# Optimization experiments

Measured on AMD Instinct MI355X. Metric: run time of the kernel, lower is better.

## Reference

```python
import jax, jax.numpy as jnp
import numpy as np

B, LAT, FCON, NCOND = 1024, 64, 256, 1
HID, E, GATE_H = 512, 8, 64
FREC, NFUT = 256, 2
IN_SZ = LAT + FCON * NCOND          # 320
INTER = LAT + HID                   # 576
OUT_SZ = NFUT * FREC                # 512


def setup_inputs() -> dict:
    key = jax.random.key(0)
    ks = jax.random.split(key, 16)

    def kaiming(k, shape):
        # kaiming_uniform over fan_in = shape[-2] (matches torch init on [E, in, out])
        fan_in = shape[-2]
        bound = np.sqrt(6.0 / fan_in)
        return jax.random.uniform(k, shape, jnp.float32, -bound, bound)

    def lin(kw, kb, din, dout):
        bound = 1.0 / np.sqrt(din)
        w = jax.random.uniform(kw, (din, dout), jnp.float32, -bound, bound)
        b = jax.random.uniform(kb, (dout,), jnp.float32, -bound, bound)
        return w, b

    gw1, gb1 = lin(ks[0], ks[1], IN_SZ, GATE_H)
    gw2, gb2 = lin(ks[2], ks[3], GATE_H, GATE_H)
    gw3, gb3 = lin(ks[4], ks[5], GATE_H, E)

    return {
        "z": jax.random.normal(ks[6], (B, LAT), jnp.float32),
        "c": jax.random.normal(ks[7], (B, FCON * NCOND), jnp.float32),
        "w0": kaiming(ks[8], (E, IN_SZ, HID)),
        "b0": jnp.full((E, HID), 0.01, jnp.float32),
        "w1": kaiming(ks[9], (E, INTER, HID)),
        "b1": jnp.full((E, HID), 0.01, jnp.float32),
        "w2": kaiming(ks[10], (E, INTER, OUT_SZ)),
        "b2": jnp.full((E, OUT_SZ), 0.01, jnp.float32),
        "gw1": gw1, "gb1": gb1,
        "gw2": gw2, "gb2": gb2,
        "gw3": gw3, "gb3": gb3,
    }


def _moe_layer(coeff, z, layer_out, w, b, act):
    # math identical to: mixed_w = coeff @ flat(w); baddbmm(mixed_b, inp, mixed_w)
    # expressed as a fused contraction (no [B, in, out] materialization)
    inp = jnp.concatenate((z, layer_out), axis=1)          # [B, in]
    out = jnp.einsum('bi,eio,be->bo', inp, w, coeff)       # [B, out]
    out = out + coeff @ b                                  # mixed bias
    return act(out) if act is not None else out


def reference(z, c, w0, b0, w1, b1, w2, b2, gw1, gb1, gw2, gb2, gw3, gb3):
    x = jnp.concatenate((z, c), axis=1)                    # [B, IN_SZ]
    h = jax.nn.elu(x @ gw1 + gb1)
    h = jax.nn.elu(h @ gw2 + gb2)
    coeff = jax.nn.softmax(h @ gw3 + gb3, axis=1)          # [B, E]

    out = _moe_layer(coeff, z, c, w0, b0, jax.nn.elu)      # [B, HID]
    out = _moe_layer(coeff, z, out, w1, b1, jax.nn.elu)    # [B, HID]
    out = _moe_layer(coeff, z, out, w2, b2, None)          # [B, OUT_SZ]
    return out
```

## Files before the change

### kernel.cpp

```cpp
#include <hip/hip_runtime.h>
#include <hip/hip_bf16.h>
#include <stdint.h>
#include <math.h>

#define B_    1024
#define LAT   64
#define FCON  256
#define IN_SZ 320
#define HID   512
#define E_    8
#define GH    64
#define INTER 576
#define OUT_SZ 512
#define NTOT  4096
#define KI0   10
#define KI12  18

typedef __attribute__((ext_vector_type(8))) __bf16 bf16x8;
typedef __attribute__((ext_vector_type(4))) float  f32x4;

__device__ __forceinline__ float elu_f(float x) { return x > 0.f ? x : expf(x) - 1.f; }
__device__ __forceinline__ __bf16 to_bf16(float f) {
    __hip_bfloat16 h = __float2bfloat16(f);
    return *reinterpret_cast<__bf16*>(&h);
}

__device__ __forceinline__ void async_ld16(const void* g, void* l) {
    __builtin_amdgcn_global_load_lds(
        (const __attribute__((address_space(1))) unsigned int*)g,
        (__attribute__((address_space(3))) unsigned int*)l,
        16, 0, 0);
}


#define PREP_GATE 64
#define PREP_ZC   (PREP_GATE + 160)
#define PREP_W0   (PREP_ZC + 8 * KI0 * 2)
#define PREP_W1   (PREP_W0 + 8 * KI12 * 2)
#define PREP_W2   (PREP_W1 + 8 * KI12 * 2)
#define PREP_ALL  PREP_W2

#define WPAD 261
#define SMEM_F (32 * WPAD)

__device__ __forceinline__ void do_zcpack(
    int bx, const float* __restrict__ z, const float* __restrict__ c,
    bf16x8* __restrict__ Ap0, bf16x8* __restrict__ Ap1, bf16x8* __restrict__ Ap2)
{
    const int wid  = bx * 4 + (threadIdx.x >> 6);
    const int lane = threadIdx.x & 63, q = lane >> 4, r = lane & 15;
    bf16x8 v;
    if (wid < 128) {
        const int mi = wid >> 1, ki = wid & 1;
        const float* src = z + (size_t)(mi * 16 + r) * LAT + ki * 32 + q * 8;
        const f32x4 lo = *(const f32x4*)src, hi = *(const f32x4*)(src + 4);
#pragma unroll
        for (int j = 0; j < 4; j++) { v[j] = to_bf16(lo[j]); v[j + 4] = to_bf16(hi[j]); }
        Ap0[((size_t)mi * KI0  + ki) * 64 + lane] = v;
        Ap1[((size_t)mi * KI12 + ki) * 64 + lane] = v;
        Ap2[((size_t)mi * KI12 + ki) * 64 + lane] = v;
    } else {
        const int cid = wid - 128;
        const int mi = cid >> 3, ki = 2 + (cid & 7);
        const float* src = c + (size_t)(mi * 16 + r) * FCON + (ki - 2) * 32 + q * 8;
        const f32x4 lo = *(const f32x4*)src, hi = *(const f32x4*)(src + 4);
#pragma unroll
        for (int j = 0; j < 4; j++) { v[j] = to_bf16(lo[j]); v[j + 4] = to_bf16(hi[j]); }
        Ap0[((size_t)mi * KI0 + ki) * 64 + lane] = v;
    }
}

__device__ __forceinline__ void do_wpack2(
    int f, const float* __restrict__ w, bf16x8* __restrict__ Wp, int KI,
    float* __restrict__ lds)
{
    const int e = f / (2 * KI), rem = f % (2 * KI);
    const int ki = rem >> 1, ot2 = rem & 1;
    const int K = KI * 32;
    const float* base = w + ((size_t)e * K + ki * 32) * 512 + ot2 * 256;

#pragma unroll
    for (int p = 0; p < 8; ++p) {
        const int idx = p * 256 + threadIdx.x;
        const int kl = idx >> 6, c4 = idx & 63;
        const f32x4 v = *(const f32x4*)(base + (size_t)kl * 512 + c4 * 4);
        float* d = lds + kl * WPAD + c4 * 4;
        d[0] = v[0]; d[1] = v[1]; d[2] = v[2]; d[3] = v[3];
    }
    __syncthreads();

    const int wv = threadIdx.x >> 6, lane = threadIdx.x & 63;
    const int q = lane >> 4, r = lane & 15;
#pragma unroll
    for (int ff = 0; ff < 4; ++ff) {
        const int fo = wv * 4 + ff;
        const int ol = fo * 16 + r;
        bf16x8 v;
#pragma unroll
        for (int j = 0; j < 8; ++j) v[j] = to_bf16(lds[(q * 8 + j) * WPAD + ol]);
        const int ni = e * 32 + ot2 * 16 + fo;
        Wp[((size_t)ni * KI + ki) * 64 + lane] = v;
    }
}

__device__ __forceinline__ void do_gate(
    int bx, const float* __restrict__ z, const float* __restrict__ c,
    const float* __restrict__ gw1, const float* __restrict__ gb1,
    const float* __restrict__ gw2, const float* __restrict__ gb2,
    const float* __restrict__ gw3, const float* __restrict__ gb3,
    float* __restrict__ coeff, float* __restrict__ smem)
{
    float* xs = smem;
    float* h  = smem + 16 * 320;
    const int r0 = bx * 16;
    const int wave = threadIdx.x >> 6, lane = threadIdx.x & 63;

#pragma unroll
    for (int p = 0; p < 5; ++p) {
        const int idx = p * 256 + threadIdx.x;
        const int row = idx / 80, c4 = idx % 80;
        const float* src = (c4 < 16)
            ? (z + (size_t)(r0 + row) * LAT  + c4 * 4)
            : (c + (size_t)(r0 + row) * FCON + (c4 - 16) * 4);
        *(f32x4*)(xs + row * 320 + c4 * 4) = *(const f32x4*)src;
    }
    __syncthreads();

    float a0, a1, a2, a3;
    {
        const float b = gb1[lane];
        a0 = b; a1 = b; a2 = b; a3 = b;
        const float* x0 = xs + (wave * 4 + 0) * 320;
        const float* x1 = xs + (wave * 4 + 1) * 320;
        const float* x2 = xs + (wave * 4 + 2) * 320;
        const float* x3 = xs + (wave * 4 + 3) * 320;
#pragma unroll 8
        for (int i = 0; i < IN_SZ; ++i) {
            const float wv = gw1[i * GH + lane];
            a0 = fmaf(x0[i], wv, a0);
            a1 = fmaf(x1[i], wv, a1);
            a2 = fmaf(x2[i], wv, a2);
            a3 = fmaf(x3[i], wv, a3);
        }
        h[(wave * 4 + 0) * GH + lane] = elu_f(a0);
        h[(wave * 4 + 1) * GH + lane] = elu_f(a1);
        h[(wave * 4 + 2) * GH + lane] = elu_f(a2);
        h[(wave * 4 + 3) * GH + lane] = elu_f(a3);
    }
    {
        const float b = gb2[lane];
        a0 = b; a1 = b; a2 = b; a3 = b;
        const float* h0 = h + (wave * 4 + 0) * GH;
        const float* h1 = h + (wave * 4 + 1) * GH;
        const float* h2 = h + (wave * 4 + 2) * GH;
        const float* h3 = h + (wave * 4 + 3) * GH;
#pragma unroll 8
        for (int i = 0; i < GH; ++i) {
            const float wv = gw2[i * GH + lane];
            a0 = fmaf(h0[i], wv, a0);
            a1 = fmaf(h1[i], wv, a1);
            a2 = fmaf(h2[i], wv, a2);
            a3 = fmaf(h3[i], wv, a3);
        }
        h[(wave * 4 + 0) * GH + lane] = elu_f(a0);
        h[(wave * 4 + 1) * GH + lane] = elu_f(a1);
        h[(wave * 4 + 2) * GH + lane] = elu_f(a2);
        h[(wave * 4 + 3) * GH + lane] = elu_f(a3);
    }
    if (lane < 32) {
        const int rloc = lane >> 3, e = lane & 7;
        const float* hr = h + (wave * 4 + rloc) * GH;
        float lg = gb3[e];
#pragma unroll 8
        for (int i = 0; i < GH; ++i) lg = fmaf(hr[i], gw3[i * E_ + e], lg);
        float mx = lg;
        mx = fmaxf(mx, __shfl_xor(mx, 1, 8));
        mx = fmaxf(mx, __shfl_xor(mx, 2, 8));
        mx = fmaxf(mx, __shfl_xor(mx, 4, 8));
        const float ex = expf(lg - mx);
        float sm = ex;
        sm += __shfl_xor(sm, 1, 8);
        sm += __shfl_xor(sm, 2, 8);
        sm += __shfl_xor(sm, 4, 8);
        coeff[(size_t)(r0 + wave * 4 + rloc) * E_ + e] = ex / sm;
    }
}

__global__ __launch_bounds__(256) void prep_kernel(
    const float* __restrict__ z, const float* __restrict__ c,
    const float* __restrict__ w0, const float* __restrict__ w1,
    const float* __restrict__ w2,
    const float* __restrict__ gw1, const float* __restrict__ gb1,
    const float* __restrict__ gw2, const float* __restrict__ gb2,
    const float* __restrict__ gw3, const float* __restrict__ gb3,
    bf16x8* __restrict__ Ap0, bf16x8* __restrict__ Ap1, bf16x8* __restrict__ Ap2,
    bf16x8* __restrict__ Wp0, bf16x8* __restrict__ Wp1, bf16x8* __restrict__ Wp2,
    float* __restrict__ coeff)
{
    __shared__ float smem[SMEM_F];
    const int bx = blockIdx.x;
    if (bx < PREP_GATE) {
        do_gate(bx, z, c, gw1, gb1, gw2, gb2, gw3, gb3, coeff, smem);
    } else if (bx < PREP_ZC) {
        do_zcpack(bx - PREP_GATE, z, c, Ap0, Ap1, Ap2);
    } else if (bx < PREP_W0) {
        do_wpack2(bx - PREP_ZC, w0, Wp0, KI0, smem);
    } else if (bx < PREP_W1) {
        do_wpack2(bx - PREP_W0, w1, Wp1, KI12, smem);
    } else {
        do_wpack2(bx - PREP_W1, w2, Wp2, KI12, smem);
    }
}

template<int KI, int FINAL>
__global__ __launch_bounds__(256) void layer_kernel(
    const bf16x8* __restrict__ Ap, const bf16x8* __restrict__ Wp,
    const float* __restrict__ coeff, const float* __restrict__ bias,
    __bf16* __restrict__ ApN, float* __restrict__ fout)
{
    constexpr int NS = KI / 2;
    __shared__ bf16x8 bs[2][2][E_][64];
    const int lane = threadIdx.x & 63, w = threadIdx.x >> 6;
    const int q = lane >> 4, r = lane & 15;
    const int o0 = blockIdx.x * 16;
    const int nt = blockIdx.x;
    const int mi = blockIdx.y * 4 + w;

    const bf16x8* aB = Ap + (size_t)mi * KI * 64 + lane;
    const int e0 = w * 2;

    f32x4 acc[E_];
#pragma unroll
    for (int e = 0; e < E_; e++) acc[e] = (f32x4){0.f, 0.f, 0.f, 0.f};

#define STAGE(s_, buf_)                                                        \
    {                                                                          \
        _Pragma("unroll")                                                      \
        for (int kk = 0; kk < 2; ++kk) {                                       \
            _Pragma("unroll")                                                  \
            for (int t = 0; t < 2; ++t) {                                      \
                const int e = e0 + t;                                          \
                const bf16x8* g = Wp +                                         \
                    ((size_t)e * 32 * KI + (size_t)nt * KI + ((s_) * 2 + kk)) * 64 + lane; \
                async_ld16((const void*)g, (void*)&bs[buf_][kk][e][0]);        \
            }                                                                  \
        }                                                                      \
    }

    STAGE(0, 0);
    bf16x8 af0 = aB[0], af1 = aB[64];
    __syncthreads();

    int cur = 0;
#pragma unroll
    for (int s = 0; s < NS; ++s) {
        bf16x8 afn0 = af0, afn1 = af1;
        if (s + 1 < NS) {
            STAGE(s + 1, cur ^ 1);
            afn0 = aB[(size_t)(s * 2 + 2) * 64];
            afn1 = aB[(size_t)(s * 2 + 3) * 64];
        }
#pragma unroll
        for (int kk = 0; kk < 2; ++kk) {
            const bf16x8 af = kk ? af1 : af0;
            bf16x8 bfr[E_];
#pragma unroll
            for (int e = 0; e < E_; e++) bfr[e] = bs[cur][kk][e][lane];
#pragma unroll
            for (int e = 0; e < E_; e++)
                acc[e] = __builtin_amdgcn_mfma_f32_16x16x32_bf16(af, bfr[e], acc[e], 0, 0, 0);
        }
        __syncthreads();
        af0 = afn0; af1 = afn1; cur ^= 1;
    }
#undef STAGE

    float be[E_];
#pragma unroll
    for (int e = 0; e < E_; e++) be[e] = bias[(size_t)e * 512 + o0 + r];

#pragma unroll
    for (int v = 0; v < 4; v++) {
        const int row = mi * 16 + q * 4 + v;
        const float* cr = coeff + (size_t)row * E_;
        const f32x4 clo = *(const f32x4*)cr, chi = *(const f32x4*)(cr + 4);
        float sv = 0.f;
#pragma unroll
        for (int e = 0; e < 4; e++) sv += clo[e] * (acc[e][v] + be[e]);
#pragma unroll
        for (int e = 0; e < 4; e++) sv += chi[e] * (acc[4 + e][v] + be[4 + e]);
        if (FINAL) {
            fout[(size_t)row * OUT_SZ + o0 + r] = sv;
        } else {
            const float hh = elu_f(sv);
            const int k  = LAT + o0 + r;
            const int ki2 = k >> 5, kq2 = (k & 31) >> 3, jb2 = k & 7;
            ApN[(((size_t)mi * KI12 + ki2) * 64 + kq2 * 16 + (q * 4 + v)) * 8 + jb2] =
                to_bf16(hh);
        }
    }
}

static inline size_t align256(size_t x) { return (x + 255) & ~(size_t)255; }

extern "C" void kernel_launch(void* const* d_in, const int* in_sizes, int n_in,
                              void* d_out, int out_size, void* d_ws, size_t ws_size,
                              hipStream_t stream)
{
    const float* z   = (const float*)d_in[0];
    const float* c   = (const float*)d_in[1];
    const float* w0  = (const float*)d_in[2];
    const float* b0  = (const float*)d_in[3];
    const float* w1  = (const float*)d_in[4];
    const float* b1  = (const float*)d_in[5];
    const float* w2  = (const float*)d_in[6];
    const float* b2  = (const float*)d_in[7];
    const float* gw1 = (const float*)d_in[8];
    const float* gb1 = (const float*)d_in[9];
    const float* gw2 = (const float*)d_in[10];
    const float* gb2 = (const float*)d_in[11];
    const float* gw3 = (const float*)d_in[12];
    const float* gb3 = (const float*)d_in[13];
    float* out = (float*)d_out;

    uint8_t* p = (uint8_t*)d_ws;
    bf16x8* Wp0 = (bf16x8*)p; p += align256((size_t)NTOT * IN_SZ * 2);
    bf16x8* Wp1 = (bf16x8*)p; p += align256((size_t)NTOT * INTER * 2);
    bf16x8* Wp2 = (bf16x8*)p; p += align256((size_t)NTOT * INTER * 2);
    bf16x8* Ap0 = (bf16x8*)p; p += align256((size_t)B_ * IN_SZ * 2);
    bf16x8* Ap1 = (bf16x8*)p; p += align256((size_t)B_ * INTER * 2);
    bf16x8* Ap2 = (bf16x8*)p; p += align256((size_t)B_ * INTER * 2);
    float* coeff = (float*)p; p += align256((size_t)B_ * E_ * 4);

    prep_kernel<<<PREP_ALL, 256, 0, stream>>>(
        z, c, w0, w1, w2, gw1, gb1, gw2, gb2, gw3, gb3,
        Ap0, Ap1, Ap2, Wp0, Wp1, Wp2, coeff);

    layer_kernel<KI0, 0><<<dim3(32, 16), 256, 0, stream>>>(
        Ap0, Wp0, coeff, b0, (__bf16*)Ap1, nullptr);
    layer_kernel<KI12, 0><<<dim3(32, 16), 256, 0, stream>>>(
        Ap1, Wp1, coeff, b1, (__bf16*)Ap2, nullptr);
    layer_kernel<KI12, 1><<<dim3(32, 16), 256, 0, stream>>>(
        Ap2, Wp2, coeff, b2, nullptr, out);
}
```

Baseline: 137.7 us.

## Overlap next-layer weight packing with current layer GEMM blocks

The prep kernel now packs only w0. Packing of w1 and w2 moves into extra blocks of the preceding layer kernels, so that weight conversion runs alongside the MoE GEMM instead of delaying it. Weight packing tiles are halved to 128 output columns to give more, smaller blocks, and launch bounds request 4 blocks per CU. The cost is a larger shared-memory footprint per layer block and possible contention between GEMM and packing blocks.

After: 137.2 us. About the same (-0.4%).

```diff
diff --git a/kernel.cpp b/kernel.cpp
--- a/kernel.cpp
+++ b/kernel.cpp
@@ -33,15 +33,8 @@
 }
 
 
-#define PREP_GATE 64
-#define PREP_ZC   (PREP_GATE + 160)
-#define PREP_W0   (PREP_ZC + 8 * KI0 * 2)
-#define PREP_W1   (PREP_W0 + 8 * KI12 * 2)
-#define PREP_W2   (PREP_W1 + 8 * KI12 * 2)
-#define PREP_ALL  PREP_W2
-
-#define WPAD 261
-#define SMEM_F (32 * WPAD)
+#define SMEM_BYTES 32768
+#define WPAD2 133
 
 __device__ __forceinline__ void do_zcpack(
     int bx, const float* __restrict__ z, const float* __restrict__ c,
@@ -70,21 +63,21 @@
     }
 }
 
-__device__ __forceinline__ void do_wpack2(
+__device__ __forceinline__ void do_wpackh(
     int f, const float* __restrict__ w, bf16x8* __restrict__ Wp, int KI,
     float* __restrict__ lds)
 {
-    const int e = f / (2 * KI), rem = f % (2 * KI);
-    const int ki = rem >> 1, ot2 = rem & 1;
+    const int e = f / (KI * 4), rem = f % (KI * 4);
+    const int ki = rem >> 2, oq = rem & 3;
     const int K = KI * 32;
-    const float* base = w + ((size_t)e * K + ki * 32) * 512 + ot2 * 256;
-
-#pragma unroll
-    for (int p = 0; p < 8; ++p) {
+    const float* base = w + ((size_t)e * K + ki * 32) * 512 + oq * 128;
+
+#pragma unroll
+    for (int p = 0; p < 4; ++p) {
         const int idx = p * 256 + threadIdx.x;
-        const int kl = idx >> 6, c4 = idx & 63;
+        const int kl = idx >> 5, c4 = idx & 31;
         const f32x4 v = *(const f32x4*)(base + (size_t)kl * 512 + c4 * 4);
-        float* d = lds + kl * WPAD + c4 * 4;
+        float* d = lds + kl * WPAD2 + c4 * 4;
         d[0] = v[0]; d[1] = v[1]; d[2] = v[2]; d[3] = v[3];
     }
     __syncthreads();
@@ -92,13 +85,13 @@
     const int wv = threadIdx.x >> 6, lane = threadIdx.x & 63;
     const int q = lane >> 4, r = lane & 15;
 #pragma unroll
-    for (int ff = 0; ff < 4; ++ff) {
-        const int fo = wv * 4 + ff;
+    for (int ff = 0; ff < 2; ++ff) {
+        const int fo = wv * 2 + ff;
         const int ol = fo * 16 + r;
         bf16x8 v;
 #pragma unroll
-        for (int j = 0; j < 8; ++j) v[j] = to_bf16(lds[(q * 8 + j) * WPAD + ol]);
-        const int ni = e * 32 + ot2 * 16 + fo;
+        for (int j = 0; j < 8; ++j) v[j] = to_bf16(lds[(q * 8 + j) * WPAD2 + ol]);
+        const int ni = e * 32 + oq * 8 + fo;
         Wp[((size_t)ni * KI + ki) * 64 + lane] = v;
     }
 }
@@ -186,45 +179,18 @@
     }
 }
 
-__global__ __launch_bounds__(256) void prep_kernel(
-    const float* __restrict__ z, const float* __restrict__ c,
-    const float* __restrict__ w0, const float* __restrict__ w1,
-    const float* __restrict__ w2,
-    const float* __restrict__ gw1, const float* __restrict__ gb1,
-    const float* __restrict__ gw2, const float* __restrict__ gb2,
-    const float* __restrict__ gw3, const float* __restrict__ gb3,
-    bf16x8* __restrict__ Ap0, bf16x8* __restrict__ Ap1, bf16x8* __restrict__ Ap2,
-    bf16x8* __restrict__ Wp0, bf16x8* __restrict__ Wp1, bf16x8* __restrict__ Wp2,
-    float* __restrict__ coeff)
-{
-    __shared__ float smem[SMEM_F];
-    const int bx = blockIdx.x;
-    if (bx < PREP_GATE) {
-        do_gate(bx, z, c, gw1, gb1, gw2, gb2, gw3, gb3, coeff, smem);
-    } else if (bx < PREP_ZC) {
-        do_zcpack(bx - PREP_GATE, z, c, Ap0, Ap1, Ap2);
-    } else if (bx < PREP_W0) {
-        do_wpack2(bx - PREP_ZC, w0, Wp0, KI0, smem);
-    } else if (bx < PREP_W1) {
-        do_wpack2(bx - PREP_W0, w1, Wp1, KI12, smem);
-    } else {
-        do_wpack2(bx - PREP_W1, w2, Wp2, KI12, smem);
-    }
-}
-
 template<int KI, int FINAL>
-__global__ __launch_bounds__(256) void layer_kernel(
-    const bf16x8* __restrict__ Ap, const bf16x8* __restrict__ Wp,
+__device__ __forceinline__ void layer_body(
+    int b, const bf16x8* __restrict__ Ap, const bf16x8* __restrict__ Wp,
     const float* __restrict__ coeff, const float* __restrict__ bias,
-    __bf16* __restrict__ ApN, float* __restrict__ fout)
+    __bf16* __restrict__ ApN, float* __restrict__ fout, bf16x8* bs)
 {
     constexpr int NS = KI / 2;
-    __shared__ bf16x8 bs[2][2][E_][64];
     const int lane = threadIdx.x & 63, w = threadIdx.x >> 6;
     const int q = lane >> 4, r = lane & 15;
-    const int o0 = blockIdx.x * 16;
-    const int nt = blockIdx.x;
-    const int mi = blockIdx.y * 4 + w;
+    const int nt = b & 31, by = b >> 5;
+    const int o0 = nt * 16;
+    const int mi = by * 4 + w;
 
     const bf16x8* aB = Ap + (size_t)mi * KI * 64 + lane;
     const int e0 = w * 2;
@@ -233,6 +199,7 @@
 #pragma unroll
     for (int e = 0; e < E_; e++) acc[e] = (f32x4){0.f, 0.f, 0.f, 0.f};
 
+#define BSI(buf_, kk_, e_) (&bs[(((size_t)(buf_) * 2 + (kk_)) * E_ + (e_)) * 64])
 #define STAGE(s_, buf_)                                                        \
     {                                                                          \
         _Pragma("unroll")                                                      \
@@ -242,7 +209,7 @@
                 const int e = e0 + t;                                          \
                 const bf16x8* g = Wp +                                         \
                     ((size_t)e * 32 * KI + (size_t)nt * KI + ((s_) * 2 + kk)) * 64 + lane; \
-                async_ld16((const void*)g, (void*)&bs[buf_][kk][e][0]);        \
+                async_ld16((const void*)g, (void*)BSI(buf_, kk, e));           \
             }                                                                  \
         }                                                                      \
     }
@@ -265,7 +232,7 @@
             const bf16x8 af = kk ? af1 : af0;
             bf16x8 bfr[E_];
 #pragma unroll
-            for (int e = 0; e < E_; e++) bfr[e] = bs[cur][kk][e][lane];
+            for (int e = 0; e < E_; e++) bfr[e] = *(BSI(cur, kk, e) + lane);
 #pragma unroll
             for (int e = 0; e < E_; e++)
                 acc[e] = __builtin_amdgcn_mfma_f32_16x16x32_bf16(af, bfr[e], acc[e], 0, 0, 0);
@@ -274,6 +241,7 @@
         af0 = afn0; af1 = afn1; cur ^= 1;
     }
 #undef STAGE
+#undef BSI
 
     float be[E_];
 #pragma unroll
@@ -298,6 +266,47 @@
             ApN[(((size_t)mi * KI12 + ki2) * 64 + kq2 * 16 + (q * 4 + v)) * 8 + jb2] =
                 to_bf16(hh);
         }
+    }
+}
+
+#define D1_GATE 64
+#define D1_ZC   (D1_GATE + 160)
+#define D1_ALL  (D1_ZC + 8 * KI0 * 4)
+
+__global__ __launch_bounds__(256, 4) void prep_kernel(
+    const float* __restrict__ z, const float* __restrict__ c,
+    const float* __restrict__ w0,
+    const float* __restrict__ gw1, const float* __restrict__ gb1,
+    const float* __restrict__ gw2, const float* __restrict__ gb2,
+    const float* __restrict__ gw3, const float* __restrict__ gb3,
+    bf16x8* __restrict__ Ap0, bf16x8* __restrict__ Ap1, bf16x8* __restrict__ Ap2,
+    bf16x8* __restrict__ Wp0,
+    float* __restrict__ coeff)
+{
+    __shared__ __align__(16) uint8_t smem[SMEM_BYTES];
+    const int bx = blockIdx.x;
+    if (bx < D1_GATE) {
+        do_gate(bx, z, c, gw1, gb1, gw2, gb2, gw3, gb3, coeff, (float*)smem);
+    } else if (bx < D1_ZC) {
+        do_zcpack(bx - D1_GATE, z, c, Ap0, Ap1, Ap2);
+    } else {
+        do_wpackh(bx - D1_ZC, w0, Wp0, KI0, (float*)smem);
+    }
+}
+
+template<int KI, int FINAL>
+__global__ __launch_bounds__(256, 4) void layer_wpack_kernel(
+    const bf16x8* __restrict__ Ap, const bf16x8* __restrict__ Wp,
+    const float* __restrict__ coeff, const float* __restrict__ bias,
+    __bf16* __restrict__ ApN, float* __restrict__ fout,
+    const float* __restrict__ wsrc, bf16x8* __restrict__ WpN)
+{
+    __shared__ __align__(16) uint8_t smem[SMEM_BYTES];
+    const int b = blockIdx.x;
+    if (b < 512) {
+        layer_body<KI, FINAL>(b, Ap, Wp, coeff, bias, ApN, fout, (bf16x8*)smem);
+    } else {
+        do_wpackh(b - 512, wsrc, WpN, KI12, (float*)smem);
     }
 }
 
@@ -332,14 +341,16 @@
     bf16x8* Ap2 = (bf16x8*)p; p += align256((size_t)B_ * INTER * 2);
     float* coeff = (float*)p; p += align256((size_t)B_ * E_ * 4);
 
-    prep_kernel<<<PREP_ALL, 256, 0, stream>>>(
-        z, c, w0, w1, w2, gw1, gb1, gw2, gb2, gw3, gb3,
-        Ap0, Ap1, Ap2, Wp0, Wp1, Wp2, coeff);
-
-    layer_kernel<KI0, 0><<<dim3(32, 16), 256, 0, stream>>>(
-        Ap0, Wp0, coeff, b0, (__bf16*)Ap1, nullptr);
-    layer_kernel<KI12, 0><<<dim3(32, 16), 256, 0, stream>>>(
-        Ap1, Wp1, coeff, b1, (__bf16*)Ap2, nullptr);
-    layer_kernel<KI12, 1><<<dim3(32, 16), 256, 0, stream>>>(
-        Ap2, Wp2, coeff, b2, nullptr, out);
-}
+    prep_kernel<<<D1_ALL, 256, 0, stream>>>(
+        z, c, w0, gw1, gb1, gw2, gb2, gw3, gb3,
+        Ap0, Ap1, Ap2, Wp0, coeff);
+
+    layer_wpack_kernel<KI0, 0><<<512 + 8 * KI12 * 4, 256, 0, stream>>>(
+        Ap0, Wp0, coeff, b0, (__bf16*)Ap1, nullptr, w1, Wp1);
+
+    layer_wpack_kernel<KI12, 0><<<512 + 8 * KI12 * 4, 256, 0, stream>>>(
+        Ap1, Wp1, coeff, b1, (__bf16*)Ap2, nullptr, w2, Wp2);
+
+    layer_wpack_kernel<KI12, 1><<<512, 256, 0, stream>>>(
+        Ap2, Wp2, coeff, b2, nullptr, out, nullptr, nullptr);
+}
```

## Fuse prep and three MoE layers into one cooperative kernel with grid syncs

Applied to the files above, without the earlier changes.

Replaces the four separate launches with one cooperative persistent kernel of 512 blocks that uses grid-wide syncs between phases. Packing of w1 and w2 weights is moved out of the prologue and overlapped with or deferred past layer 0. The aim is to cut launch gaps and tail effects between the small kernels. The cost is grid.sync overhead, and the whole grid must be co-resident, with a fallback to the old multi-kernel path if the cooperative launch fails.

Measured after the change: 492.4 us. +257.7%, slower.

```diff
diff --git a/kernel.cpp b/kernel.cpp
--- a/kernel.cpp
+++ b/kernel.cpp
@@ -1,7 +1,10 @@
 #include <hip/hip_runtime.h>
+#include <hip/hip_cooperative_groups.h>
 #include <hip/hip_bf16.h>
 #include <stdint.h>
 #include <math.h>
+
+namespace cg = cooperative_groups;
 
 #define B_    1024
 #define LAT   64
@@ -32,13 +35,6 @@
         16, 0, 0);
 }
 
-
-#define PREP_GATE 64
-#define PREP_ZC   (PREP_GATE + 160)
-#define PREP_W0   (PREP_ZC + 8 * KI0 * 2)
-#define PREP_W1   (PREP_W0 + 8 * KI12 * 2)
-#define PREP_W2   (PREP_W1 + 8 * KI12 * 2)
-#define PREP_ALL  PREP_W2
 
 #define WPAD 261
 #define SMEM_F (32 * WPAD)
@@ -186,6 +182,151 @@
     }
 }
 
+template<int KI, int FINAL>
+__device__ __forceinline__ void layer_body(
+    int b, const bf16x8* __restrict__ Ap, const bf16x8* __restrict__ Wp,
+    const float* __restrict__ coeff, const float* __restrict__ bias,
+    __bf16* __restrict__ ApN, float* __restrict__ fout, bf16x8* bs)
+{
+    constexpr int NS = KI / 2;
+    const int lane = threadIdx.x & 63, w = threadIdx.x >> 6;
+    const int q = lane >> 4, r = lane & 15;
+    const int nt = b & 31, by = b >> 5;
+    const int o0 = nt * 16;
+    const int mi = by * 4 + w;
+
+    const bf16x8* aB = Ap + (size_t)mi * KI * 64 + lane;
+    const int e0 = w * 2;
+
+    f32x4 acc[E_];
+#pragma unroll
+    for (int e = 0; e < E_; e++) acc[e] = (f32x4){0.f, 0.f, 0.f, 0.f};
+
+#define BSI(buf_, kk_, e_) (&bs[(((size_t)(buf_) * 2 + (kk_)) * E_ + (e_)) * 64])
+#define STAGE(s_, buf_)                                                        \
+    {                                                                          \
+        _Pragma("unroll")                                                      \
+        for (int kk = 0; kk < 2; ++kk) {                                       \
+            _Pragma("unroll")                                                  \
+            for (int t = 0; t < 2; ++t) {                                      \
+                const int e = e0 + t;                                          \
+                const bf16x8* g = Wp +                                         \
+                    ((size_t)e * 32 * KI + (size_t)nt * KI + ((s_) * 2 + kk)) * 64 + lane; \
+                async_ld16((const void*)g, (void*)BSI(buf_, kk, e));           \
+            }                                                                  \
+        }                                                                      \
+    }
+
+    STAGE(0, 0);
+    bf16x8 af0 = aB[0], af1 = aB[64];
+    __syncthreads();
+
+    int cur = 0;
+#pragma unroll
+    for (int s = 0; s < NS; ++s) {
+        bf16x8 afn0 = af0, afn1 = af1;
+        if (s + 1 < NS) {
+            STAGE(s + 1, cur ^ 1);
+            afn0 = aB[(size_t)(s * 2 + 2) * 64];
+            afn1 = aB[(size_t)(s * 2 + 3) * 64];
+        }
+#pragma unroll
+        for (int kk = 0; kk < 2; ++kk) {
+            const bf16x8 af = kk ? af1 : af0;
+            bf16x8 bfr[E_];
+#pragma unroll
+            for (int e = 0; e < E_; e++) bfr[e] = *(BSI(cur, kk, e) + lane);
+#pragma unroll
+            for (int e = 0; e < E_; e++)
+                acc[e] = __builtin_amdgcn_mfma_f32_16x16x32_bf16(af, bfr[e], acc[e], 0, 0, 0);
+        }
+        __syncthreads();
+        af0 = afn0; af1 = afn1; cur ^= 1;
+    }
+#undef STAGE
+#undef BSI
+
+    float be[E_];
+#pragma unroll
+    for (int e = 0; e < E_; e++) be[e] = bias[(size_t)e * 512 + o0 + r];
+
+#pragma unroll
+    for (int v = 0; v < 4; v++) {
+        const int row = mi * 16 + q * 4 + v;
+        const float* cr = coeff + (size_t)row * E_;
+        const f32x4 clo = *(const f32x4*)cr, chi = *(const f32x4*)(cr + 4);
+        float sv = 0.f;
+#pragma unroll
+        for (int e = 0; e < 4; e++) sv += clo[e] * (acc[e][v] + be[e]);
+#pragma unroll
+        for (int e = 0; e < 4; e++) sv += chi[e] * (acc[4 + e][v] + be[4 + e]);
+        if (FINAL) {
+            fout[(size_t)row * OUT_SZ + o0 + r] = sv;
+        } else {
+            const float hh = elu_f(sv);
+            const int k  = LAT + o0 + r;
+            const int ki2 = k >> 5, kq2 = (k & 31) >> 3, jb2 = k & 7;
+            ApN[(((size_t)mi * KI12 + ki2) * 64 + kq2 * 16 + (q * 4 + v)) * 8 + jb2] =
+                to_bf16(hh);
+        }
+    }
+}
+
+__global__ __launch_bounds__(256, 2) void fused_kernel(
+    const float* __restrict__ z, const float* __restrict__ c,
+    const float* __restrict__ w0, const float* __restrict__ b0,
+    const float* __restrict__ w1, const float* __restrict__ b1,
+    const float* __restrict__ w2, const float* __restrict__ b2,
+    const float* __restrict__ gw1, const float* __restrict__ gb1,
+    const float* __restrict__ gw2, const float* __restrict__ gb2,
+    const float* __restrict__ gw3, const float* __restrict__ gb3,
+    bf16x8* __restrict__ Ap0, bf16x8* __restrict__ Ap1, bf16x8* __restrict__ Ap2,
+    bf16x8* __restrict__ Wp0, bf16x8* __restrict__ Wp1, bf16x8* __restrict__ Wp2,
+    float* __restrict__ coeff, float* __restrict__ out)
+{
+    __shared__ __align__(16) float smem[SMEM_F];
+    cg::grid_group grid = cg::this_grid();
+    const int b = blockIdx.x;
+
+    if (b < 64) {
+        do_gate(b, z, c, gw1, gb1, gw2, gb2, gw3, gb3, coeff, smem);
+    } else if (b < 224) {
+        do_zcpack(b - 64, z, c, Ap0, Ap1, Ap2);
+    } else if (b < 384) {
+        do_wpack2(b - 224, w0, Wp0, KI0, smem);
+    } else {
+        do_wpack2(b - 384, w1, Wp1, KI12, smem);
+    }
+    __threadfence();
+    grid.sync();
+
+    layer_body<KI0, 0>(b, Ap0, Wp0, coeff, b0, (__bf16*)Ap1, nullptr,
+                       (bf16x8*)smem);
+    __syncthreads();
+    if (b < 160) {
+        do_wpack2(128 + b, w1, Wp1, KI12, smem);
+    } else if (b < 448) {
+        do_wpack2(b - 160, w2, Wp2, KI12, smem);
+    }
+    __threadfence();
+    grid.sync();
+
+    layer_body<KI12, 0>(b, Ap1, Wp1, coeff, b1, (__bf16*)Ap2, nullptr,
+                        (bf16x8*)smem);
+    __threadfence();
+    grid.sync();
+
+    layer_body<KI12, 1>(b, Ap2, Wp2, coeff, b2, nullptr, out,
+                        (bf16x8*)smem);
+}
+
+#define PREP_GATE 64
+#define PREP_ZC   (PREP_GATE + 160)
+#define PREP_W0   (PREP_ZC + 8 * KI0 * 2)
+#define PREP_W1   (PREP_W0 + 8 * KI12 * 2)
+#define PREP_W2   (PREP_W1 + 8 * KI12 * 2)
+#define PREP_ALL  PREP_W2
+
 __global__ __launch_bounds__(256) void prep_kernel(
     const float* __restrict__ z, const float* __restrict__ c,
     const float* __restrict__ w0, const float* __restrict__ w1,
@@ -197,7 +338,7 @@
     bf16x8* __restrict__ Wp0, bf16x8* __restrict__ Wp1, bf16x8* __restrict__ Wp2,
     float* __restrict__ coeff)
 {
-    __shared__ float smem[SMEM_F];
+    __shared__ __align__(16) float smem[SMEM_F];
     const int bx = blockIdx.x;
     if (bx < PREP_GATE) {
         do_gate(bx, z, c, gw1, gb1, gw2, gb2, gw3, gb3, coeff, smem);
@@ -218,87 +359,9 @@
     const float* __restrict__ coeff, const float* __restrict__ bias,
     __bf16* __restrict__ ApN, float* __restrict__ fout)
 {
-    constexpr int NS = KI / 2;
-    __shared__ bf16x8 bs[2][2][E_][64];
-    const int lane = threadIdx.x & 63, w = threadIdx.x >> 6;
-    const int q = lane >> 4, r = lane & 15;
-    const int o0 = blockIdx.x * 16;
-    const int nt = blockIdx.x;
-    const int mi = blockIdx.y * 4 + w;
-
-    const bf16x8* aB = Ap + (size_t)mi * KI * 64 + lane;
-    const int e0 = w * 2;
-
-    f32x4 acc[E_];
-#pragma unroll
-    for (int e = 0; e < E_; e++) acc[e] = (f32x4){0.f, 0.f, 0.f, 0.f};
-
-#define STAGE(s_, buf_)                                                        \
-    {                                                                          \
-        _Pragma("unroll")                                                      \
-        for (int kk = 0; kk < 2; ++kk) {                                       \
-            _Pragma("unroll")                                                  \
-            for (int t = 0; t < 2; ++t) {                                      \
-                const int e = e0 + t;                                          \
-                const bf16x8* g = Wp +                                         \
-                    ((size_t)e * 32 * KI + (size_t)nt * KI + ((s_) * 2 + kk)) * 64 + lane; \
-                async_ld16((const void*)g, (void*)&bs[buf_][kk][e][0]);        \
-            }                                                                  \
-        }                                                                      \
-    }
-
-    STAGE(0, 0);
-    bf16x8 af0 = aB[0], af1 = aB[64];
-    __syncthreads();
-
-    int cur = 0;
-#pragma unroll
-    for (int s = 0; s < NS; ++s) {
-        bf16x8 afn0 = af0, afn1 = af1;
-        if (s + 1 < NS) {
-            STAGE(s + 1, cur ^ 1);
-            afn0 = aB[(size_t)(s * 2 + 2) * 64];
-            afn1 = aB[(size_t)(s * 2 + 3) * 64];
-        }
-#pragma unroll
-        for (int kk = 0; kk < 2; ++kk) {
-            const bf16x8 af = kk ? af1 : af0;
-            bf16x8 bfr[E_];
-#pragma unroll
-            for (int e = 0; e < E_; e++) bfr[e] = bs[cur][kk][e][lane];
-#pragma unroll
-            for (int e = 0; e < E_; e++)
-                acc[e] = __builtin_amdgcn_mfma_f32_16x16x32_bf16(af, bfr[e], acc[e], 0, 0, 0);
-        }
-        __syncthreads();
-        af0 = afn0; af1 = afn1; cur ^= 1;
-    }
-#undef STAGE
-
-    float be[E_];
-#pragma unroll
-    for (int e = 0; e < E_; e++) be[e] = bias[(size_t)e * 512 + o0 + r];
-
-#pragma unroll
-    for (int v = 0; v < 4; v++) {
-        const int row = mi * 16 + q * 4 + v;
-        const float* cr = coeff + (size_t)row * E_;
-        const f32x4 clo = *(const f32x4*)cr, chi = *(const f32x4*)(cr + 4);
-        float sv = 0.f;
-#pragma unroll
-        for (int e = 0; e < 4; e++) sv += clo[e] * (acc[e][v] + be[e]);
-#pragma unroll
-        for (int e = 0; e < 4; e++) sv += chi[e] * (acc[4 + e][v] + be[4 + e]);
-        if (FINAL) {
-            fout[(size_t)row * OUT_SZ + o0 + r] = sv;
-        } else {
-            const float hh = elu_f(sv);
-            const int k  = LAT + o0 + r;
-            const int ki2 = k >> 5, kq2 = (k & 31) >> 3, jb2 = k & 7;
-            ApN[(((size_t)mi * KI12 + ki2) * 64 + kq2 * 16 + (q * 4 + v)) * 8 + jb2] =
-                to_bf16(hh);
-        }
-    }
+    __shared__ __align__(16) bf16x8 bs[2 * 2 * E_ * 64];
+    layer_body<KI, FINAL>(blockIdx.y * 32 + blockIdx.x,
+                          Ap, Wp, coeff, bias, ApN, fout, bs);
 }
 
 static inline size_t align256(size_t x) { return (x + 255) & ~(size_t)255; }
@@ -332,14 +395,25 @@
     bf16x8* Ap2 = (bf16x8*)p; p += align256((size_t)B_ * INTER * 2);
     float* coeff = (float*)p; p += align256((size_t)B_ * E_ * 4);
 
-    prep_kernel<<<PREP_ALL, 256, 0, stream>>>(
-        z, c, w0, w1, w2, gw1, gb1, gw2, gb2, gw3, gb3,
-        Ap0, Ap1, Ap2, Wp0, Wp1, Wp2, coeff);
-
-    layer_kernel<KI0, 0><<<dim3(32, 16), 256, 0, stream>>>(
-        Ap0, Wp0, coeff, b0, (__bf16*)Ap1, nullptr);
-    layer_kernel<KI12, 0><<<dim3(32, 16), 256, 0, stream>>>(
-        Ap1, Wp1, coeff, b1, (__bf16*)Ap2, nullptr);
-    layer_kernel<KI12, 1><<<dim3(32, 16), 256, 0, stream>>>(
-        Ap2, Wp2, coeff, b2, nullptr, out);
-}
+    void* args[] = {
+        (void*)&z, (void*)&c,
+        (void*)&w0, (void*)&b0, (void*)&w1, (void*)&b1, (void*)&w2, (void*)&b2,
+        (void*)&gw1, (void*)&gb1, (void*)&gw2, (void*)&gb2, (void*)&gw3, (void*)&gb3,
+        (void*)&Ap0, (void*)&Ap1, (void*)&Ap2,
+        (void*)&Wp0, (void*)&Wp1, (void*)&Wp2,
+        (void*)&coeff, (void*)&out,
+    };
+    hipError_t rc = hipLaunchCooperativeKernel((const void*)fused_kernel,
+                                               dim3(512), dim3(256), args, 0, stream);
+    if (rc != hipSuccess) {
+        prep_kernel<<<PREP_ALL, 256, 0, stream>>>(
+            z, c, w0, w1, w2, gw1, gb1, gw2, gb2, gw3, gb3,
+            Ap0, Ap1, Ap2, Wp0, Wp1, Wp2, coeff);
+        layer_kernel<KI0, 0><<<dim3(32, 16), 256, 0, stream>>>(
+            Ap0, Wp0, coeff, b0, (__bf16*)Ap1, nullptr);
+        layer_kernel<KI12, 0><<<dim3(32, 16), 256, 0, stream>>>(
+            Ap1, Wp1, coeff, b1, (__bf16*)Ap2, nullptr);
+        layer_kernel<KI12, 1><<<dim3(32, 16), 256, 0, stream>>>(
+            Ap2, Wp2, coeff, b2, nullptr, out);
+    }
+}
```
